# Kernel tuning notes

Hardware: AMD Instinct MI355X
Metric: run time of the kernel (lower is better)

Reference implementation:

```python
import jax, jax.numpy as jnp
import numpy as np

N_NODES = 50000
N_EDGES = 1600000
IN_DIM, HID_DIM, OUT_DIM = 512, 256, 128
N_IDX = 8192


def _graph_conv(x, src, dst, W, b, n_nodes):
    # DGL GraphConv, norm='both': D_dst^{-1/2} A D_src^{-1/2} x W + b
    ones = jnp.ones(src.shape[0], dtype=x.dtype)
    deg_out = jax.ops.segment_sum(ones, src, num_segments=n_nodes)
    deg_in = jax.ops.segment_sum(ones, dst, num_segments=n_nodes)
    ns = jax.lax.rsqrt(jnp.maximum(deg_out, 1.0))  # source norm
    nd = jax.lax.rsqrt(jnp.maximum(deg_in, 1.0))   # dest norm
    msg = (x * ns[:, None])[src]                   # gather [E, F]
    agg = jax.ops.segment_sum(msg, dst, num_segments=n_nodes)
    return (agg * nd[:, None]) @ W + b


def _gcn(x, src, dst, W1, b1, W2, b2, n_nodes):
    h = jax.nn.relu(_graph_conv(x, src, dst, W1, b1, n_nodes))
    return _graph_conv(h, src, dst, W2, b2, n_nodes)


def setup_inputs() -> dict:
    key = jax.random.key(0)
    ks = jax.random.split(key, 16)
    d = {
        'raw1': jax.random.normal(ks[0], (N_NODES, IN_DIM), jnp.float32),
        'raw2': jax.random.normal(ks[1], (N_NODES, IN_DIM), jnp.float32),
        'src1': jax.random.randint(ks[2], (N_EDGES,), 0, N_NODES),
        'dst1': jax.random.randint(ks[3], (N_EDGES,), 0, N_NODES),
        'src2': jax.random.randint(ks[4], (N_EDGES,), 0, N_NODES),
        'dst2': jax.random.randint(ks[5], (N_EDGES,), 0, N_NODES),
        'index': jax.random.randint(ks[6], (N_IDX,), 0, N_NODES),
    }
    def lin(k, fi, fo):
        s = 1.0 / np.sqrt(fi)
        return jax.random.uniform(k, (fi, fo), jnp.float32, -s, s)
    d['e1_W1'] = lin(ks[7], IN_DIM, HID_DIM); d['e1_b1'] = jnp.zeros(HID_DIM, jnp.float32)
    d['e1_W2'] = lin(ks[8], HID_DIM, OUT_DIM); d['e1_b2'] = jnp.zeros(OUT_DIM, jnp.float32)
    d['e2_W1'] = lin(ks[9], IN_DIM, HID_DIM); d['e2_b1'] = jnp.zeros(HID_DIM, jnp.float32)
    d['e2_W2'] = lin(ks[10], HID_DIM, OUT_DIM); d['e2_b2'] = jnp.zeros(OUT_DIM, jnp.float32)
    return d


def reference(raw1, raw2, src1, dst1, src2, dst2, index,
              e1_W1, e1_b1, e1_W2, e1_b2, e2_W1, e2_b1, e2_W2, e2_b2):
    n = raw1.shape[0]
    c1 = _gcn(raw1, src1, dst1, e1_W1, e1_b1, e1_W2, e1_b2, n)[index]
    c2 = _gcn(raw2, src2, dst2, e2_W1, e2_b1, e2_W2, e2_b2, n)[index]
    # F.normalize(dim=1), eps=1e-12
    c1 = c1 / jnp.maximum(jnp.linalg.norm(c1, axis=1, keepdims=True), 1e-12)
    c2 = c2 / jnp.maximum(jnp.linalg.norm(c2, axis=1, keepdims=True), 1e-12)
    z1 = c1 @ c1.T
    z2 = c2 @ c2.T
    z3 = c1 @ c2.T
    z3 = (z3 + z3.T) * 0.5
    z = (z1 + z2 + z3) * (1.0 / 3.0)
    return jnp.triu(z)
```

## Files before the change

### kernel.cpp

```cpp
#include <hip/hip_runtime.h>
#include <hip/hip_bf16.h>

using u16 = unsigned short;
using u32 = unsigned int;

typedef __attribute__((ext_vector_type(8))) short short8;
typedef __attribute__((ext_vector_type(4))) float f32x4;

__device__ __forceinline__ u16 f2bf_u16(float f) {
    __hip_bfloat16 h = __float2bfloat16(f);
    return __builtin_bit_cast(u16, h);
}
__device__ __forceinline__ float bfu(u32 u) { return __uint_as_float(u << 16); }

static constexpr int NN = 50000;
static constexpr int NE = 1600000;
static constexpr int NIDX = 8192;
static constexpr int NRANGE = 8;
static constexpr int RN = NN / NRANGE;
static constexpr int HCH = 16;
static constexpr int NK = NN * NRANGE;
static constexpr int SAB = (NK + 4095) / 4096;
static constexpr int CAPB = 262144;
static constexpr int PEB = 8192;
static constexpr int PGX = (NE + PEB - 1) / PEB;
static constexpr int PSTG = 1536;
static constexpr int ZLB = 64 * 63 / 2;
static constexpr int ZHB = ZLB / 2;
static constexpr int ZUB = 64 * 65 / 2;
static constexpr int AGB = NN / 4;


__global__ __launch_bounds__(256)
void partition_kernel(const int* __restrict__ s1, const int* __restrict__ d1,
                      const int* __restrict__ s2, const int* __restrict__ d2,
                      int* __restrict__ bcur, u32* __restrict__ ebuf_d, u16* __restrict__ ebuf_s) {
    __shared__ u32 stage_d[8][PSTG];
    __shared__ u16 stage_s[8][PSTG];
    __shared__ int cnt_d[8], cnt_s[8], base_d[8], base_s[8];
    int enc = blockIdx.y;
    const int* s = enc ? s2 : s1;
    const int* d = enc ? d2 : d1;
    if (threadIdx.x < 8) { cnt_d[threadIdx.x] = 0; cnt_s[threadIdx.x] = 0; }
    __syncthreads();
    int* bc_d = bcur + enc * 16;
    int* bc_s = bcur + enc * 16 + 8;
    u32* bd = ebuf_d + (size_t)enc * 8 * CAPB;
    u16* bs = ebuf_s + (size_t)enc * 8 * CAPB;
    int e0 = blockIdx.x * PEB;
    int e1 = min(e0 + PEB, NE);
    for (int e = e0 + threadIdx.x * 4; e < e1; e += 1024) {
        int4 sv = *(const int4*)(s + e);
        int4 dv = *(const int4*)(d + e);
        #pragma unroll
        for (int j = 0; j < 4; ++j) {
            int src = j == 0 ? sv.x : j == 1 ? sv.y : j == 2 ? sv.z : sv.w;
            int dst = j == 0 ? dv.x : j == 1 ? dv.y : j == 2 ? dv.z : dv.w;
            int rd = dst / RN;
            u32 entry = (u32)src | ((u32)(dst - rd * RN) << 16);
            int slot = atomicAdd(&cnt_d[rd], 1);
            if (slot < PSTG) stage_d[rd][slot] = entry;
            else { int gp = atomicAdd(&bc_d[rd], 1); bd[(size_t)rd * CAPB + gp] = entry; }
            int rs = src / RN;
            int slot2 = atomicAdd(&cnt_s[rs], 1);
            if (slot2 < PSTG) stage_s[rs][slot2] = (u16)(src - rs * RN);
            else { int gp = atomicAdd(&bc_s[rs], 1); bs[(size_t)rs * CAPB + gp] = (u16)(src - rs * RN); }
        }
    }
    __syncthreads();
    if (threadIdx.x < 8) {
        int b = threadIdx.x;
        base_d[b] = atomicAdd(&bc_d[b], min(cnt_d[b], PSTG));
        base_s[b] = atomicAdd(&bc_s[b], min(cnt_s[b], PSTG));
    }
    __syncthreads();
    #pragma unroll
    for (int b = 0; b < 8; ++b) {
        int nb = min(cnt_d[b], PSTG);
        for (int i = threadIdx.x; i < nb; i += 256)
            bd[(size_t)b * CAPB + base_d[b] + i] = stage_d[b][i];
        int ns = min(cnt_s[b], PSTG);
        for (int i = threadIdx.x; i < ns; i += 256)
            bs[(size_t)b * CAPB + base_s[b] + i] = stage_s[b][i];
    }
}


__global__ __launch_bounds__(256)
void bhist_kernel(const u32* __restrict__ ebuf_d, const u16* __restrict__ ebuf_s,
                  const int* __restrict__ bcur,
                  u32* __restrict__ partial2, u32* __restrict__ partial_out) {
    __shared__ u32 sh[RN * 2];
    int stripe = blockIdx.x & 7, chunk = blockIdx.x >> 3;
    int enc = blockIdx.y & 1, type = blockIdx.y >> 1;
    if (type == 0) {
        for (int i = threadIdx.x; i < RN * 2; i += 256) sh[i] = 0;
        __syncthreads();
        int size = bcur[enc * 16 + stripe];
        int cs = (size + HCH - 1) / HCH;
        int lo = chunk * cs, hi = min(lo + cs, size);
        const u32* b = ebuf_d + ((size_t)enc * 8 + stripe) * CAPB;
        for (int i = lo + threadIdx.x; i < hi; i += 256) {
            u32 e = b[i];
            u32 idx = (e >> 16) * 8 + (e & 0xffffu) / RN;
            atomicAdd(&sh[idx >> 2], 1u << ((idx & 3) * 8));
        }
        __syncthreads();
        u32* p2 = partial2 + ((size_t)enc * HCH + chunk) * (NN * 2) + stripe * (RN * 2);
        for (int i = threadIdx.x; i < RN * 2; i += 256) p2[i] = sh[i];
    } else {
        for (int i = threadIdx.x; i < RN / 2; i += 256) sh[i] = 0;
        __syncthreads();
        int size = bcur[enc * 16 + 8 + stripe];
        int cs = (size + HCH - 1) / HCH;
        int lo = chunk * cs, hi = min(lo + cs, size);
        const u16* b = ebuf_s + ((size_t)enc * 8 + stripe) * CAPB;
        for (int i = lo + threadIdx.x; i < hi; i += 256) {
            u32 sl = b[i];
            atomicAdd(&sh[sl >> 1], 1u << ((sl & 1) * 16));
        }
        __syncthreads();
        u32* po = partial_out + ((size_t)enc * HCH + chunk) * (NN / 2) + stripe * (RN / 2);
        for (int i = threadIdx.x; i < RN / 2; i += 256) po[i] = sh[i];
    }
}

__global__ void reduce_hist_kernel(const u32* __restrict__ partial2,
                                   const u32* __restrict__ partial_out,
                                   int* __restrict__ deg2, float* __restrict__ norms) {
    int i = blockIdx.x * blockDim.x + threadIdx.x;
    if (i >= 2 * NN) return;
    int enc = i / NN;
    int dst = i - enc * NN;
    int cnt[8];
    #pragma unroll
    for (int r = 0; r < 8; ++r) cnt[r] = 0;
    for (int c = 0; c < HCH; ++c) {
        const u32* p = partial2 + ((size_t)enc * HCH + c) * (NN * 2) + dst * 2;
        u32 w0 = p[0], w1 = p[1];
        cnt[0] += w0 & 0xff; cnt[1] += (w0 >> 8) & 0xff; cnt[2] += (w0 >> 16) & 0xff; cnt[3] += w0 >> 24;
        cnt[4] += w1 & 0xff; cnt[5] += (w1 >> 8) & 0xff; cnt[6] += (w1 >> 16) & 0xff; cnt[7] += w1 >> 24;
    }
    int* dp = deg2 + (size_t)enc * NK + dst * 8;
    int din = 0;
    #pragma unroll
    for (int r = 0; r < 8; ++r) { dp[r] = cnt[r]; din += cnt[r]; }
    norms[(enc * 2 + 1) * NN + dst] = rsqrtf(fmaxf((float)din, 1.f));
    int dout = 0;
    for (int c = 0; c < HCH; ++c) {
        u32 w = partial_out[((size_t)enc * HCH + c) * (NN / 2) + (dst >> 1)];
        dout += (w >> ((dst & 1) * 16)) & 0xffff;
    }
    norms[(enc * 2 + 0) * NN + dst] = rsqrtf(fmaxf((float)dout, 1.f));
}


__global__ __launch_bounds__(1024)
void scanA_kernel(const int* __restrict__ deg2, int* __restrict__ rp2_all, int* __restrict__ tot) {
    int enc = blockIdx.y;
    const int* deg = deg2 + (size_t)enc * NK;
    int* rp = rp2_all + (size_t)enc * (NK + 1);
    __shared__ int wsum[16];
    int t = threadIdx.x, lane = t & 63, wid = t >> 6;
    int i0 = blockIdx.x * 4096 + t * 4;
    int4 v = make_int4(0, 0, 0, 0);
    bool in = (i0 + 3 < NK);
    if (in) v = *(const int4*)(deg + i0);
    int s = v.x + v.y + v.z + v.w;
    int x = s;
    #pragma unroll
    for (int d = 1; d < 64; d <<= 1) {
        int y = __shfl_up(x, d, 64);
        if (lane >= d) x += y;
    }
    if (lane == 63) wsum[wid] = x;
    __syncthreads();
    if (t == 0) {
        int run = 0;
        #pragma unroll
        for (int w = 0; w < 16; ++w) { int q = wsum[w]; wsum[w] = run; run += q; }
        tot[enc * SAB + blockIdx.x] = run;
    }
    __syncthreads();
    if (in) {
        int excl = wsum[wid] + x - s;
        rp[i0] = excl;
        rp[i0 + 1] = excl + v.x;
        rp[i0 + 2] = excl + v.x + v.y;
        rp[i0 + 3] = excl + v.x + v.y + v.z;
    }
}

__global__ __launch_bounds__(256)
void scanC_kernel(int* __restrict__ rp2_all, int* __restrict__ cur2_all, const int* __restrict__ tot) {
    int enc = blockIdx.y;
    int* rp = rp2_all + (size_t)enc * (NK + 1);
    int* cur = cur2_all + (size_t)enc * NK;
    int nA = blockIdx.x >> 2;
    int part = 0;
    for (int i = threadIdx.x; i < nA; i += 256) part += tot[enc * SAB + i];
    #pragma unroll
    for (int d = 1; d < 64; d <<= 1) part += __shfl_xor(part, d, 64);
    __shared__ int red[4];
    __shared__ int soff;
    int lane = threadIdx.x & 63, wv = threadIdx.x >> 6;
    if (lane == 0) red[wv] = part;
    __syncthreads();
    if (threadIdx.x == 0) soff = red[0] + red[1] + red[2] + red[3];
    __syncthreads();
    int off = soff;
    int idx = (blockIdx.x * 256 + threadIdx.x) * 4;
    if (idx < NK) {
        int4 v = *(const int4*)(rp + idx);
        v.x += off; v.y += off; v.z += off; v.w += off;
        *(int4*)(rp + idx) = v;
        *(int4*)(cur + idx) = v;
    }
    if (blockIdx.x == 0 && threadIdx.x == 0) rp[NK] = NE;
}


__global__ __launch_bounds__(256)
void scatter_kernel(const u32* __restrict__ ebuf_d, const int* __restrict__ bcur,
                    int* __restrict__ cur2_all, u16* __restrict__ csr_all) {
    int stripe = blockIdx.x & 7, chunk = blockIdx.x >> 3;
    int enc = blockIdx.y;
    int size = bcur[enc * 16 + stripe];
    int cs = (size + 63) / 64;
    int lo = chunk * cs, hi = min(lo + cs, size);
    const u32* b = ebuf_d + ((size_t)enc * 8 + stripe) * CAPB;
    int* cursor = cur2_all + (size_t)enc * NK;
    u16* csr = csr_all + (size_t)enc * NE;
    int base = stripe * RN;
    for (int i = lo + threadIdx.x; i < hi; i += 256) {
        u32 e = b[i];
        int src = e & 0xffff;
        int dst = base + (int)(e >> 16);
        int key = dst * 8 + src / RN;
        int pos = atomicAdd(&cursor[key], 1);
        csr[pos] = (u16)src;
    }
}

__global__ void convw_kernel(const float* __restrict__ W1a, const float* __restrict__ W1b,
                             const float* __restrict__ W2a, const float* __restrict__ W2b,
                             u16* __restrict__ W1t_all, u16* __restrict__ W2t_all) {
    int mat = blockIdx.y;
    int idx = blockIdx.x * blockDim.x + threadIdx.x;
    const float* W; u16* Wt; int K, N;
    if (mat < 2) { W = mat ? W1b : W1a; Wt = W1t_all + (size_t)mat * 512 * 256; K = 512; N = 256; }
    else         { W = (mat == 3) ? W2b : W2a; Wt = W2t_all + (size_t)(mat - 2) * 256 * 128; K = 256; N = 128; }
    if (idx < K * N) {
        int k = idx / N, n = idx - k * N;
        Wt[(size_t)n * K + k] = f2bf_u16(W[idx]);
    }
}


template<bool A_F32, bool OUT_BF16, bool TRIANG, bool SCALE>
__global__ __launch_bounds__(256)
void gemm_kernel(const void* __restrict__ A0_, const void* __restrict__ A1_,
                 const u16* __restrict__ Bt0, const u16* __restrict__ Bt1,
                 void* __restrict__ C0_, void* __restrict__ C1_,
                 const float* __restrict__ rs0, const float* __restrict__ rs1,
                 int M, int N, int K) {
    int enc = blockIdx.z;
    const void* A_ = enc ? A1_ : A0_;
    const u16* Bt = enc ? Bt1 : Bt0;
    void* C_ = enc ? C1_ : C0_;
    const float* rowscale = enc ? rs1 : rs0;

    int it, jt;
    if (TRIANG) {
        int b = blockIdx.x;
        int i = (int)((129.0f - sqrtf(129.f * 129.f - 8.f * b)) * 0.5f);
        while ((i + 1) * (129 - (i + 1)) / 2 <= b) ++i;
        while (i * (129 - i) / 2 > b) --i;
        it = i;
        jt = i + (b - i * (129 - i) / 2);
    } else {
        it = blockIdx.x; jt = blockIdx.y;
    }
    int t = threadIdx.x;
    int brow = it * 128, bcol = jt * 128;
    float* Cf = (float*)C_;
    __shared__ alignas(16) u16 smem[128 * 40 * 2];
    u16* As = smem;
    u16* Bs = smem + 128 * 40;
    int lane = t & 63, wv = t >> 6;
    int wr = wv >> 1, wc = wv & 1;
    f32x4 acc[4][4];
    #pragma unroll
    for (int m = 0; m < 4; ++m)
        #pragma unroll
        for (int n = 0; n < 4; ++n) acc[m][n] = f32x4{0.f, 0.f, 0.f, 0.f};

    float4 a_f0[4], a_f1[4];
    uint4  a_h0[2], a_h1[2];
    uint4  b_h0[2], b_h1[2];

#define LOADT(S, kk) do {                                                          \
    if constexpr (A_F32) {                                                         \
        const float* A = (const float*)A_;                                         \
        _Pragma("unroll")                                                          \
        for (int p = 0; p < 4; ++p) {                                              \
            int r = p * 32 + (t >> 3), c = (t & 7) * 4;                            \
            int gr = brow + r;                                                     \
            a_f##S[p] = make_float4(0.f, 0.f, 0.f, 0.f);                           \
            if (gr < M) a_f##S[p] = *(const float4*)(A + (size_t)gr * K + (kk) + c); \
        }                                                                          \
    } else {                                                                       \
        const u16* A = (const u16*)A_;                                             \
        _Pragma("unroll")                                                          \
        for (int p = 0; p < 2; ++p) {                                              \
            int r = p * 64 + (t >> 2), c = (t & 3) * 8;                            \
            int gr = brow + r;                                                     \
            a_h##S[p] = make_uint4(0u, 0u, 0u, 0u);                                \
            if (gr < M) a_h##S[p] = *(const uint4*)(A + (size_t)gr * K + (kk) + c); \
        }                                                                          \
    }                                                                              \
    _Pragma("unroll")                                                              \
    for (int p = 0; p < 2; ++p) {                                                  \
        int r = p * 64 + (t >> 2), c = (t & 3) * 8;                                \
        int gn = bcol + r;                                                         \
        b_h##S[p] = make_uint4(0u, 0u, 0u, 0u);                                    \
        if (gn < N) b_h##S[p] = *(const uint4*)(Bt + (size_t)gn * K + (kk) + c);   \
    }                                                                              \
} while (0)

#define STORET(S) do {                                                             \
    if constexpr (A_F32) {                                                         \
        _Pragma("unroll")                                                          \
        for (int p = 0; p < 4; ++p) {                                              \
            int r = p * 32 + (t >> 3), c = (t & 7) * 4;                            \
            u32 lo = (u32)f2bf_u16(a_f##S[p].x) | ((u32)f2bf_u16(a_f##S[p].y) << 16); \
            u32 hi = (u32)f2bf_u16(a_f##S[p].z) | ((u32)f2bf_u16(a_f##S[p].w) << 16); \
            *(uint2*)&As[r * 40 + c] = make_uint2(lo, hi);                         \
        }                                                                          \
    } else {                                                                       \
        _Pragma("unroll")                                                          \
        for (int p = 0; p < 2; ++p) {                                              \
            int r = p * 64 + (t >> 2), c = (t & 3) * 8;                            \
            *(uint4*)&As[r * 40 + c] = a_h##S[p];                                  \
        }                                                                          \
    }                                                                              \
    _Pragma("unroll")                                                              \
    for (int p = 0; p < 2; ++p) {                                                  \
        int r = p * 64 + (t >> 2), c = (t & 3) * 8;                                \
        *(uint4*)&Bs[r * 40 + c] = b_h##S[p];                                      \
    }                                                                              \
} while (0)

    auto compute = [&]() {
        int kg = (lane >> 4) * 8;
        short8 av[4], bv[4];
        #pragma unroll
        for (int m = 0; m < 4; ++m)
            av[m] = *(const short8*)&As[(wr * 64 + m * 16 + (lane & 15)) * 40 + kg];
        #pragma unroll
        for (int n = 0; n < 4; ++n)
            bv[n] = *(const short8*)&Bs[(wc * 64 + n * 16 + (lane & 15)) * 40 + kg];
        #pragma unroll
        for (int m = 0; m < 4; ++m)
            #pragma unroll
            for (int n = 0; n < 4; ++n)
                acc[m][n] = __builtin_amdgcn_mfma_f32_16x16x32_bf16(av[m], bv[n], acc[m][n], 0, 0, 0);
    };

    LOADT(0, 0);
    LOADT(1, 32);
    for (int k0 = 0; k0 < K; k0 += 64) {
        STORET(0);
        __syncthreads();
        if (k0 + 64 < K) LOADT(0, k0 + 64);
        compute();
        __syncthreads();
        STORET(1);
        __syncthreads();
        if (k0 + 96 < K) LOADT(1, k0 + 96);
        compute();
        __syncthreads();
    }
#undef LOADT
#undef STORET

    const int lane15 = lane & 15, lanehi = lane >> 4;
    if (OUT_BF16) {
        u16* stg = smem + wv * 1024;
        #pragma unroll
        for (int m = 0; m < 4; ++m) {
            #pragma unroll
            for (int n = 0; n < 4; ++n)
                #pragma unroll
                for (int r = 0; r < 4; ++r) {
                    float v = acc[m][n][r];
                    if (SCALE) v *= rowscale[brow + wr * 64 + m * 16 + lanehi * 4 + r];
                    stg[(lanehi * 4 + r) * 64 + n * 16 + lane15] = f2bf_u16(v);
                }
            #pragma unroll
            for (int pass = 0; pass < 2; ++pass) {
                int lr = pass * 8 + (lane >> 3);
                int grow = brow + wr * 64 + m * 16 + lr;
                uint4 w = *(uint4*)&stg[lr * 64 + (lane & 7) * 8];
                if (grow < M)
                    *(uint4*)((u16*)C_ + (size_t)grow * N + bcol + wc * 64 + (lane & 7) * 8) = w;
            }
        }
    } else {
        float* stg = (float*)smem + wv * 1024;
        #pragma unroll
        for (int m = 0; m < 4; ++m) {
            #pragma unroll
            for (int n = 0; n < 4; ++n)
                #pragma unroll
                for (int r = 0; r < 4; ++r) {
                    int row = brow + wr * 64 + m * 16 + lanehi * 4 + r;
                    int col = bcol + wc * 64 + n * 16 + lane15;
                    float v = acc[m][n][r];
                    if (SCALE) v *= rowscale[row];
                    if (TRIANG && col < row) v = 0.f;
                    stg[(lanehi * 4 + r) * 64 + n * 16 + lane15] = v;
                }
            #pragma unroll
            for (int pass = 0; pass < 4; ++pass) {
                int lr = pass * 4 + lanehi;
                int grow = brow + wr * 64 + m * 16 + lr;
                f32x4 w = *(f32x4*)&stg[lr * 64 + lane15 * 4];
                if (grow < M) {
                    float* dp = Cf + (size_t)grow * N + bcol + wc * 64 + lane15 * 4;
                    if (TRIANG) __builtin_nontemporal_store(w, (f32x4*)dp);
                    else *(f32x4*)dp = w;
                }
            }
        }
    }
}


template<int F, bool RELU, bool OUT_BF16, bool ZFILL>
__global__ __launch_bounds__(256)
void agg_kernel(const u16* __restrict__ Yall, const int* __restrict__ rp2_all,
                const u16* __restrict__ csr_all, const float* __restrict__ norms,
                const float* __restrict__ bias0, const float* __restrict__ bias1,
                void* __restrict__ out_all, float* __restrict__ zout) {
    constexpr int VPL = F / 64;
    int enc = blockIdx.y;
    int bid = blockIdx.x;
    if (ZFILL) {
        if (bid < ZHB) {
            int b = enc * ZHB + bid;
            float fit = (sqrtf(8.f * b + 1.f) + 1.f) * 0.5f;
            int it = (int)fit;
            if (it * (it - 1) / 2 > b) --it;
            else if ((it + 1) * it / 2 <= b) ++it;
            int jt = b - it * (it - 1) / 2;
            int brow = it * 128, bcol = jt * 128;
            f32x4 z = {0.f, 0.f, 0.f, 0.f};
            #pragma unroll
            for (int pq = 0; pq < 16; ++pq) {
                int idx = pq * 256 + threadIdx.x;
                int r = idx >> 5, c4 = idx & 31;
                __builtin_nontemporal_store(z, (f32x4*)(zout + (size_t)(brow + r) * NIDX + bcol + c4 * 4));
            }
            return;
        }
        bid -= ZHB;
    }
    const u16* Y = Yall + (size_t)enc * NN * F;
    const int* rp2 = rp2_all + (size_t)enc * (NK + 1);
    const u16* csr = csr_all + (size_t)enc * NE;
    const float* nd = norms + (size_t)(2 * enc + 1) * NN;
    const float* bias = enc ? bias1 : bias0;
    int lane = threadIdx.x & 63;
    int node = bid * 4 + (threadIdx.x >> 6);
    int e0 = rp2[node * 8], e1 = rp2[node * 8 + 8];
    float acc[VPL];
    #pragma unroll
    for (int j = 0; j < VPL; ++j) acc[j] = 0.f;
    const int off = lane * VPL;

    int e = e0;
    for (; e < e1 && (e & 7) != 0; ++e) {
        int s = csr[e];
        if (VPL == 4) {
            uint2 d = *(const uint2*)(Y + (size_t)s * F + off);
            acc[0] += bfu(d.x & 0xffffu); acc[1] += bfu(d.x >> 16);
            acc[2] += bfu(d.y & 0xffffu); acc[3] += bfu(d.y >> 16);
        } else {
            u32 d = *(const u32*)(Y + (size_t)s * F + off);
            acc[0] += bfu(d & 0xffffu); acc[1] += bfu(d >> 16);
        }
    }
    if (VPL == 4) {
        for (; e + 16 <= e1; e += 16) {
            uint4 ia = *(const uint4*)(csr + e);
            uint4 ib = *(const uint4*)(csr + e + 8);
            int s0 = ia.x & 0xffff, s1 = ia.x >> 16, s2 = ia.y & 0xffff, s3 = ia.y >> 16;
            int s4 = ia.z & 0xffff, s5 = ia.z >> 16, s6 = ia.w & 0xffff, s7 = ia.w >> 16;
            int s8 = ib.x & 0xffff, s9 = ib.x >> 16, sa = ib.y & 0xffff, sb = ib.y >> 16;
            int sc = ib.z & 0xffff, sd = ib.z >> 16, se = ib.w & 0xffff, sf = ib.w >> 16;
            uint2 d0 = *(const uint2*)(Y + (size_t)s0 * F + off);
            uint2 d1 = *(const uint2*)(Y + (size_t)s1 * F + off);
            uint2 d2 = *(const uint2*)(Y + (size_t)s2 * F + off);
            uint2 d3 = *(const uint2*)(Y + (size_t)s3 * F + off);
            uint2 d4 = *(const uint2*)(Y + (size_t)s4 * F + off);
            uint2 d5 = *(const uint2*)(Y + (size_t)s5 * F + off);
            uint2 d6 = *(const uint2*)(Y + (size_t)s6 * F + off);
            uint2 d7 = *(const uint2*)(Y + (size_t)s7 * F + off);
            uint2 d8 = *(const uint2*)(Y + (size_t)s8 * F + off);
            uint2 d9 = *(const uint2*)(Y + (size_t)s9 * F + off);
            uint2 da = *(const uint2*)(Y + (size_t)sa * F + off);
            uint2 db = *(const uint2*)(Y + (size_t)sb * F + off);
            uint2 dc = *(const uint2*)(Y + (size_t)sc * F + off);
            uint2 dd = *(const uint2*)(Y + (size_t)sd * F + off);
            uint2 de = *(const uint2*)(Y + (size_t)se * F + off);
            uint2 df = *(const uint2*)(Y + (size_t)sf * F + off);
            acc[0] += bfu(d0.x & 0xffffu); acc[1] += bfu(d0.x >> 16); acc[2] += bfu(d0.y & 0xffffu); acc[3] += bfu(d0.y >> 16);
            acc[0] += bfu(d1.x & 0xffffu); acc[1] += bfu(d1.x >> 16); acc[2] += bfu(d1.y & 0xffffu); acc[3] += bfu(d1.y >> 16);
            acc[0] += bfu(d2.x & 0xffffu); acc[1] += bfu(d2.x >> 16); acc[2] += bfu(d2.y & 0xffffu); acc[3] += bfu(d2.y >> 16);
            acc[0] += bfu(d3.x & 0xffffu); acc[1] += bfu(d3.x >> 16); acc[2] += bfu(d3.y & 0xffffu); acc[3] += bfu(d3.y >> 16);
            acc[0] += bfu(d4.x & 0xffffu); acc[1] += bfu(d4.x >> 16); acc[2] += bfu(d4.y & 0xffffu); acc[3] += bfu(d4.y >> 16);
            acc[0] += bfu(d5.x & 0xffffu); acc[1] += bfu(d5.x >> 16); acc[2] += bfu(d5.y & 0xffffu); acc[3] += bfu(d5.y >> 16);
            acc[0] += bfu(d6.x & 0xffffu); acc[1] += bfu(d6.x >> 16); acc[2] += bfu(d6.y & 0xffffu); acc[3] += bfu(d6.y >> 16);
            acc[0] += bfu(d7.x & 0xffffu); acc[1] += bfu(d7.x >> 16); acc[2] += bfu(d7.y & 0xffffu); acc[3] += bfu(d7.y >> 16);
            acc[0] += bfu(d8.x & 0xffffu); acc[1] += bfu(d8.x >> 16); acc[2] += bfu(d8.y & 0xffffu); acc[3] += bfu(d8.y >> 16);
            acc[0] += bfu(d9.x & 0xffffu); acc[1] += bfu(d9.x >> 16); acc[2] += bfu(d9.y & 0xffffu); acc[3] += bfu(d9.y >> 16);
            acc[0] += bfu(da.x & 0xffffu); acc[1] += bfu(da.x >> 16); acc[2] += bfu(da.y & 0xffffu); acc[3] += bfu(da.y >> 16);
            acc[0] += bfu(db.x & 0xffffu); acc[1] += bfu(db.x >> 16); acc[2] += bfu(db.y & 0xffffu); acc[3] += bfu(db.y >> 16);
            acc[0] += bfu(dc.x & 0xffffu); acc[1] += bfu(dc.x >> 16); acc[2] += bfu(dc.y & 0xffffu); acc[3] += bfu(dc.y >> 16);
            acc[0] += bfu(dd.x & 0xffffu); acc[1] += bfu(dd.x >> 16); acc[2] += bfu(dd.y & 0xffffu); acc[3] += bfu(dd.y >> 16);
            acc[0] += bfu(de.x & 0xffffu); acc[1] += bfu(de.x >> 16); acc[2] += bfu(de.y & 0xffffu); acc[3] += bfu(de.y >> 16);
            acc[0] += bfu(df.x & 0xffffu); acc[1] += bfu(df.x >> 16); acc[2] += bfu(df.y & 0xffffu); acc[3] += bfu(df.y >> 16);
        }
    }
    for (; e + 8 <= e1; e += 8) {
        uint4 iv = *(const uint4*)(csr + e);
        int s0 = iv.x & 0xffff, s1 = iv.x >> 16;
        int s2 = iv.y & 0xffff, s3 = iv.y >> 16;
        int s4 = iv.z & 0xffff, s5 = iv.z >> 16;
        int s6 = iv.w & 0xffff, s7 = iv.w >> 16;
        if (VPL == 4) {
            uint2 d0 = *(const uint2*)(Y + (size_t)s0 * F + off);
            uint2 d1 = *(const uint2*)(Y + (size_t)s1 * F + off);
            uint2 d2 = *(const uint2*)(Y + (size_t)s2 * F + off);
            uint2 d3 = *(const uint2*)(Y + (size_t)s3 * F + off);
            uint2 d4 = *(const uint2*)(Y + (size_t)s4 * F + off);
            uint2 d5 = *(const uint2*)(Y + (size_t)s5 * F + off);
            uint2 d6 = *(const uint2*)(Y + (size_t)s6 * F + off);
            uint2 d7 = *(const uint2*)(Y + (size_t)s7 * F + off);
            acc[0] += bfu(d0.x & 0xffffu); acc[1] += bfu(d0.x >> 16); acc[2] += bfu(d0.y & 0xffffu); acc[3] += bfu(d0.y >> 16);
            acc[0] += bfu(d1.x & 0xffffu); acc[1] += bfu(d1.x >> 16); acc[2] += bfu(d1.y & 0xffffu); acc[3] += bfu(d1.y >> 16);
            acc[0] += bfu(d2.x & 0xffffu); acc[1] += bfu(d2.x >> 16); acc[2] += bfu(d2.y & 0xffffu); acc[3] += bfu(d2.y >> 16);
            acc[0] += bfu(d3.x & 0xffffu); acc[1] += bfu(d3.x >> 16); acc[2] += bfu(d3.y & 0xffffu); acc[3] += bfu(d3.y >> 16);
            acc[0] += bfu(d4.x & 0xffffu); acc[1] += bfu(d4.x >> 16); acc[2] += bfu(d4.y & 0xffffu); acc[3] += bfu(d4.y >> 16);
            acc[0] += bfu(d5.x & 0xffffu); acc[1] += bfu(d5.x >> 16); acc[2] += bfu(d5.y & 0xffffu); acc[3] += bfu(d5.y >> 16);
            acc[0] += bfu(d6.x & 0xffffu); acc[1] += bfu(d6.x >> 16); acc[2] += bfu(d6.y & 0xffffu); acc[3] += bfu(d6.y >> 16);
            acc[0] += bfu(d7.x & 0xffffu); acc[1] += bfu(d7.x >> 16); acc[2] += bfu(d7.y & 0xffffu); acc[3] += bfu(d7.y >> 16);
        } else {
            u32 d0 = *(const u32*)(Y + (size_t)s0 * F + off);
            u32 d1 = *(const u32*)(Y + (size_t)s1 * F + off);
            u32 d2 = *(const u32*)(Y + (size_t)s2 * F + off);
            u32 d3 = *(const u32*)(Y + (size_t)s3 * F + off);
            u32 d4 = *(const u32*)(Y + (size_t)s4 * F + off);
            u32 d5 = *(const u32*)(Y + (size_t)s5 * F + off);
            u32 d6 = *(const u32*)(Y + (size_t)s6 * F + off);
            u32 d7 = *(const u32*)(Y + (size_t)s7 * F + off);
            acc[0] += bfu(d0 & 0xffffu); acc[1] += bfu(d0 >> 16);
            acc[0] += bfu(d1 & 0xffffu); acc[1] += bfu(d1 >> 16);
            acc[0] += bfu(d2 & 0xffffu); acc[1] += bfu(d2 >> 16);
            acc[0] += bfu(d3 & 0xffffu); acc[1] += bfu(d3 >> 16);
            acc[0] += bfu(d4 & 0xffffu); acc[1] += bfu(d4 >> 16);
            acc[0] += bfu(d5 & 0xffffu); acc[1] += bfu(d5 >> 16);
            acc[0] += bfu(d6 & 0xffffu); acc[1] += bfu(d6 >> 16);
            acc[0] += bfu(d7 & 0xffffu); acc[1] += bfu(d7 >> 16);
        }
    }
    for (; e < e1; ++e) {
        int s = csr[e];
        if (VPL == 4) {
            uint2 d = *(const uint2*)(Y + (size_t)s * F + off);
            acc[0] += bfu(d.x & 0xffffu); acc[1] += bfu(d.x >> 16);
            acc[2] += bfu(d.y & 0xffffu); acc[3] += bfu(d.y >> 16);
        } else {
            u32 d = *(const u32*)(Y + (size_t)s * F + off);
            acc[0] += bfu(d & 0xffffu); acc[1] += bfu(d >> 16);
        }
    }

    float ndv = nd[node];
    #pragma unroll
    for (int j = 0; j < VPL; ++j) {
        float o = acc[j] * ndv + bias[off + j];
        if (RELU) o = fmaxf(o, 0.f);
        if (OUT_BF16) ((u16*)out_all)[(size_t)enc * NN * F + (size_t)node * F + off + j] = f2bf_u16(o);
        else ((float*)out_all)[(size_t)enc * NN * F + (size_t)node * F + off + j] = o;
    }
}


__global__ __launch_bounds__(256)
void build_r_kernel(const float* __restrict__ H2a, const float* __restrict__ H2b,
                    const int* __restrict__ index, u16* __restrict__ R) {
    int lane = threadIdx.x & 63;
    int row = blockIdx.x * 4 + (threadIdx.x >> 6);
    int g = index[row];
    float2 a = *(const float2*)(H2a + (size_t)g * 128 + lane * 2);
    float2 b = *(const float2*)(H2b + (size_t)g * 128 + lane * 2);
    float sa = a.x * a.x + a.y * a.y;
    float sb = b.x * b.x + b.y * b.y;
    #pragma unroll
    for (int d = 1; d < 64; d <<= 1) {
        sa += __shfl_xor(sa, d, 64);
        sb += __shfl_xor(sb, d, 64);
    }
    float inva = 1.f / fmaxf(sqrtf(sa), 1e-12f);
    float invb = 1.f / fmaxf(sqrtf(sb), 1e-12f);
    float ax = a.x * inva, ay = a.y * inva;
    float bx = b.x * invb, by = b.y * invb;
    const float c2 = 0.5f, c3 = 0.28867513459481287f;
    u16* Rp = R + (size_t)row * 256;
    Rp[lane * 2]           = f2bf_u16((ax + bx) * c2);
    Rp[lane * 2 + 1]       = f2bf_u16((ay + by) * c2);
    Rp[128 + lane * 2]     = f2bf_u16((ax - bx) * c3);
    Rp[128 + lane * 2 + 1] = f2bf_u16((ay - by) * c3);
}


extern "C" void kernel_launch(void* const* d_in, const int* in_sizes, int n_in,
                              void* d_out, int out_size, void* d_ws, size_t ws_size,
                              hipStream_t stream) {
    (void)in_sizes; (void)n_in; (void)out_size; (void)ws_size;
    const float* raw0 = (const float*)d_in[0];
    const float* raw1 = (const float*)d_in[1];
    const int* src1 = (const int*)d_in[2], *dst1 = (const int*)d_in[3];
    const int* src2 = (const int*)d_in[4], *dst2 = (const int*)d_in[5];
    const int* index = (const int*)d_in[6];
    const float* W1a = (const float*)d_in[7];  const float* b1a = (const float*)d_in[8];
    const float* W2a = (const float*)d_in[9];  const float* b2a = (const float*)d_in[10];
    const float* W1b = (const float*)d_in[11]; const float* b1b = (const float*)d_in[12];
    const float* W2b = (const float*)d_in[13]; const float* b2b = (const float*)d_in[14];

    char* wp = (char*)d_ws;
    auto alloc = [&](size_t bytes) -> char* {
        char* r = wp;
        wp += (bytes + 255) & ~(size_t)255;
        return r;
    };
    float* norms   = (float*)alloc((size_t)4 * NN * 4);
    int*   deg2    = (int*)alloc((size_t)2 * NK * 4);
    int*   rp2     = (int*)alloc((size_t)2 * (NK + 1) * 4);
    int*   cur2    = (int*)alloc((size_t)2 * NK * 4);
    int*   tot     = (int*)alloc((size_t)2 * SAB * 4);
    int*   bcur    = (int*)alloc(32 * 4);
    u16*   csr_all = (u16*)alloc((size_t)2 * NE * 2);
    u16*   W1t     = (u16*)alloc((size_t)2 * 512 * 256 * 2);
    u16*   W2t     = (u16*)alloc((size_t)2 * 256 * 128 * 2);
    u16*   Y1      = (u16*)alloc((size_t)2 * NN * 256 * 2);
    u16*   H1      = (u16*)alloc((size_t)2 * NN * 256 * 2);
    u16*   Y2      = (u16*)alloc((size_t)2 * NN * 128 * 2);
    float* H2      = (float*)alloc((size_t)2 * NN * 128 * 4);
    u16*   R       = (u16*)alloc((size_t)NIDX * 256 * 2);
    u32* partial2    = (u32*)Y1;
    u32* partial_out = (u32*)H1;
    u32* ebuf_d      = (u32*)Y2;
    u16* ebuf_s      = (u16*)H2;

    const int MT = (NN + 127) / 128;

    hipMemsetAsync(bcur, 0, 32 * 4, stream);
    convw_kernel<<<dim3((512 * 256 + 255) / 256, 4), 256, 0, stream>>>(W1a, W1b, W2a, W2b, W1t, W2t);
    partition_kernel<<<dim3(PGX, 2), 256, 0, stream>>>(src1, dst1, src2, dst2, bcur, ebuf_d, ebuf_s);
    bhist_kernel<<<dim3(8 * HCH, 4), 256, 0, stream>>>(ebuf_d, ebuf_s, bcur, partial2, partial_out);
    reduce_hist_kernel<<<(2 * NN + 255) / 256, 256, 0, stream>>>(partial2, partial_out, deg2, norms);
    scanA_kernel<<<dim3(SAB, 2), 1024, 0, stream>>>(deg2, rp2, tot);
    scanC_kernel<<<dim3((NK / 4 + 255) / 256, 2), 256, 0, stream>>>(rp2, cur2, tot);
    scatter_kernel<<<dim3(8 * 64, 2), 256, 0, stream>>>(ebuf_d, bcur, cur2, csr_all);

    gemm_kernel<true, true, false, true><<<dim3(MT, 2, 2), 256, 0, stream>>>(
        raw0, raw1, W1t, W1t + (size_t)512 * 256, Y1, Y1 + (size_t)NN * 256,
        norms, norms + (size_t)2 * NN, NN, 256, 512);
    agg_kernel<256, true, true, true><<<dim3(ZHB + AGB, 2), 256, 0, stream>>>(
        Y1, rp2, csr_all, norms, b1a, b1b, H1, (float*)d_out);
    gemm_kernel<false, true, false, true><<<dim3(MT, 1, 2), 256, 0, stream>>>(
        H1, H1 + (size_t)NN * 256, W2t, W2t + (size_t)256 * 128, Y2, Y2 + (size_t)NN * 128,
        norms, norms + (size_t)2 * NN, NN, 128, 256);
    agg_kernel<128, false, false, false><<<dim3(AGB, 2), 256, 0, stream>>>(
        Y2, rp2, csr_all, norms, b2a, b2b, H2, nullptr);

    build_r_kernel<<<NIDX / 4, 256, 0, stream>>>(H2, H2 + (size_t)NN * 128, index, R);
    gemm_kernel<false, false, true, false><<<dim3(ZUB, 1, 1), 256, 0, stream>>>(
        R, R, R, R, (float*)d_out, (float*)d_out, nullptr, nullptr, NIDX, NIDX, 256);
}
```

Baseline: 658.9 us.

## Fold weight conversion into partition and overlap CSR scatter with first GEMM

Weight transposition/bf16 conversion now runs on extra blocks of the partition kernel, which removes one launch. The CSR scatter runs as extra blocks appended to the first-layer GEMM grid, so it overlaps with that GEMM. Those blocks claim work through an atomic ticket counter, and the memset now also zeroes the ticket counters. The scatter's atomics and writes now compete with the GEMM for bandwidth, and the GEMM is refactored into a device function used by three kernels.

```diff
diff --git a/kernel.cpp b/kernel.cpp
--- a/kernel.cpp
+++ b/kernel.cpp
@@ -24,17 +24,44 @@
 static constexpr int CAPB = 262144;
 static constexpr int PEB = 8192;
 static constexpr int PGX = (NE + PEB - 1) / PEB;
+static constexpr int CVB = 640;
 static constexpr int PSTG = 1536;
 static constexpr int ZLB = 64 * 63 / 2;
 static constexpr int ZHB = ZLB / 2;
 static constexpr int ZUB = 64 * 65 / 2;
 static constexpr int AGB = NN / 4;
+static constexpr int MT = (NN + 127) / 128;
+static constexpr int SCX = 256;
 
 
 __global__ __launch_bounds__(256)
 void partition_kernel(const int* __restrict__ s1, const int* __restrict__ d1,
                       const int* __restrict__ s2, const int* __restrict__ d2,
-                      int* __restrict__ bcur, u32* __restrict__ ebuf_d, u16* __restrict__ ebuf_s) {
+                      int* __restrict__ bcur, u32* __restrict__ ebuf_d, u16* __restrict__ ebuf_s,
+                      const float* __restrict__ W1a, const float* __restrict__ W1b,
+                      const float* __restrict__ W2a, const float* __restrict__ W2b,
+                      u16* __restrict__ W1t, u16* __restrict__ W2t) {
+    if (blockIdx.x >= PGX) {
+        int o = (blockIdx.x - PGX) + CVB * blockIdx.y;
+        int idx = o * 256 + threadIdx.x;
+        if (idx < 131072) {
+            int k = idx >> 8, n = idx & 255;
+            W1t[(size_t)n * 512 + k] = f2bf_u16(W1a[idx]);
+        } else if (idx < 262144) {
+            int j = idx - 131072;
+            int k = j >> 8, n = j & 255;
+            W1t[(size_t)131072 + (size_t)n * 512 + k] = f2bf_u16(W1b[j]);
+        } else if (idx < 294912) {
+            int j = idx - 262144;
+            int k = j >> 7, n = j & 127;
+            W2t[(size_t)n * 256 + k] = f2bf_u16(W2a[j]);
+        } else if (idx < 327680) {
+            int j = idx - 294912;
+            int k = j >> 7, n = j & 127;
+            W2t[(size_t)32768 + (size_t)n * 256 + k] = f2bf_u16(W2b[j]);
+        }
+        return;
+    }
     __shared__ u32 stage_d[8][PSTG];
     __shared__ u16 stage_s[8][PSTG];
     __shared__ int cnt_d[8], cnt_s[8], base_d[8], base_s[8];
@@ -220,11 +247,10 @@
 }
 
 
-__global__ __launch_bounds__(256)
-void scatter_kernel(const u32* __restrict__ ebuf_d, const int* __restrict__ bcur,
-                    int* __restrict__ cur2_all, u16* __restrict__ csr_all) {
-    int stripe = blockIdx.x & 7, chunk = blockIdx.x >> 3;
-    int enc = blockIdx.y;
+__device__ __forceinline__ void scatter_body(const u32* __restrict__ ebuf_d,
+                                             const int* __restrict__ bcur,
+                                             int* __restrict__ cur2_all, u16* __restrict__ csr_all,
+                                             int stripe, int chunk, int enc) {
     int size = bcur[enc * 16 + stripe];
     int cs = (size + 63) / 64;
     int lo = chunk * cs, hi = min(lo + cs, size);
@@ -242,49 +268,14 @@
     }
 }
 
-__global__ void convw_kernel(const float* __restrict__ W1a, const float* __restrict__ W1b,
-                             const float* __restrict__ W2a, const float* __restrict__ W2b,
-                             u16* __restrict__ W1t_all, u16* __restrict__ W2t_all) {
-    int mat = blockIdx.y;
-    int idx = blockIdx.x * blockDim.x + threadIdx.x;
-    const float* W; u16* Wt; int K, N;
-    if (mat < 2) { W = mat ? W1b : W1a; Wt = W1t_all + (size_t)mat * 512 * 256; K = 512; N = 256; }
-    else         { W = (mat == 3) ? W2b : W2a; Wt = W2t_all + (size_t)(mat - 2) * 256 * 128; K = 256; N = 128; }
-    if (idx < K * N) {
-        int k = idx / N, n = idx - k * N;
-        Wt[(size_t)n * K + k] = f2bf_u16(W[idx]);
-    }
-}
-
 
 template<bool A_F32, bool OUT_BF16, bool TRIANG, bool SCALE>
-__global__ __launch_bounds__(256)
-void gemm_kernel(const void* __restrict__ A0_, const void* __restrict__ A1_,
-                 const u16* __restrict__ Bt0, const u16* __restrict__ Bt1,
-                 void* __restrict__ C0_, void* __restrict__ C1_,
-                 const float* __restrict__ rs0, const float* __restrict__ rs1,
-                 int M, int N, int K) {
-    int enc = blockIdx.z;
-    const void* A_ = enc ? A1_ : A0_;
-    const u16* Bt = enc ? Bt1 : Bt0;
-    void* C_ = enc ? C1_ : C0_;
-    const float* rowscale = enc ? rs1 : rs0;
-
-    int it, jt;
-    if (TRIANG) {
-        int b = blockIdx.x;
-        int i = (int)((129.0f - sqrtf(129.f * 129.f - 8.f * b)) * 0.5f);
-        while ((i + 1) * (129 - (i + 1)) / 2 <= b) ++i;
-        while (i * (129 - i) / 2 > b) --i;
-        it = i;
-        jt = i + (b - i * (129 - i) / 2);
-    } else {
-        it = blockIdx.x; jt = blockIdx.y;
-    }
+__device__ __forceinline__ void gemm_device(const void* __restrict__ A_, const u16* __restrict__ Bt,
+                                            void* __restrict__ C_, const float* __restrict__ rowscale,
+                                            int M, int N, int K, int it, int jt, u16* smem) {
     int t = threadIdx.x;
     int brow = it * 128, bcol = jt * 128;
     float* Cf = (float*)C_;
-    __shared__ alignas(16) u16 smem[128 * 40 * 2];
     u16* As = smem;
     u16* Bs = smem + 128 * 40;
     int lane = t & 63, wv = t >> 6;
@@ -434,6 +425,53 @@
             }
         }
     }
+}
+
+__global__ __launch_bounds__(256)
+void gemm1scat_kernel(const float* __restrict__ raw0, const float* __restrict__ raw1,
+                      const u16* __restrict__ W1t, u16* __restrict__ Y1,
+                      const float* __restrict__ norms,
+                      const u32* __restrict__ ebuf_d, const int* __restrict__ bcur,
+                      int* __restrict__ tick, int* __restrict__ cur2, u16* __restrict__ csr_all) {
+    if (blockIdx.x >= MT) {
+        u32 lin = blockIdx.x + gridDim.x * (blockIdx.y + gridDim.y * blockIdx.z);
+        int stripe = lin & 7;
+        __shared__ int tsh;
+        if (threadIdx.x == 0) tsh = atomicAdd(&tick[stripe], 1);
+        __syncthreads();
+        int tkt = tsh;
+        scatter_body(ebuf_d, bcur, cur2, csr_all, stripe, tkt & 63, tkt >> 6);
+        return;
+    }
+    __shared__ alignas(16) u16 smem[128 * 40 * 2];
+    int enc = blockIdx.z;
+    gemm_device<true, true, false, true>(
+        enc ? raw1 : raw0, W1t + (size_t)enc * 512 * 256,
+        Y1 + (size_t)enc * NN * 256, norms + (size_t)2 * enc * NN,
+        NN, 256, 512, blockIdx.x, blockIdx.y, smem);
+}
+
+__global__ __launch_bounds__(256)
+void gemm2_kernel(const u16* __restrict__ H1, const u16* __restrict__ W2t,
+                  u16* __restrict__ Y2, const float* __restrict__ norms) {
+    __shared__ alignas(16) u16 smem[128 * 40 * 2];
+    int enc = blockIdx.z;
+    gemm_device<false, true, false, true>(
+        H1 + (size_t)enc * NN * 256, W2t + (size_t)enc * 256 * 128,
+        Y2 + (size_t)enc * NN * 128, norms + (size_t)2 * enc * NN,
+        NN, 128, 256, blockIdx.x, 0, smem);
+}
+
+__global__ __launch_bounds__(256)
+void zgemm_kernel(const u16* __restrict__ R, float* __restrict__ out) {
+    int b = blockIdx.x;
+    int i = (int)((129.0f - sqrtf(129.f * 129.f - 8.f * b)) * 0.5f);
+    while ((i + 1) * (129 - (i + 1)) / 2 <= b) ++i;
+    while (i * (129 - i) / 2 > b) --i;
+    int it = i;
+    int jt = i + (b - i * (129 - i) / 2);
+    __shared__ alignas(16) u16 smem[128 * 40 * 2];
+    gemm_device<false, false, true, false>(R, R, out, nullptr, NIDX, NIDX, 256, it, jt, smem);
 }
 
 
@@ -651,7 +689,7 @@
     int*   rp2     = (int*)alloc((size_t)2 * (NK + 1) * 4);
     int*   cur2    = (int*)alloc((size_t)2 * NK * 4);
     int*   tot     = (int*)alloc((size_t)2 * SAB * 4);
-    int*   bcur    = (int*)alloc(32 * 4);
+    int*   bcur    = (int*)alloc(48 * 4);
     u16*   csr_all = (u16*)alloc((size_t)2 * NE * 2);
     u16*   W1t     = (u16*)alloc((size_t)2 * 512 * 256 * 2);
     u16*   W2t     = (u16*)alloc((size_t)2 * 256 * 128 * 2);
@@ -660,34 +698,28 @@
     u16*   Y2      = (u16*)alloc((size_t)2 * NN * 128 * 2);
     float* H2      = (float*)alloc((size_t)2 * NN * 128 * 4);
     u16*   R       = (u16*)alloc((size_t)NIDX * 256 * 2);
+    int*   tick    = bcur + 32;
     u32* partial2    = (u32*)Y1;
     u32* partial_out = (u32*)H1;
     u32* ebuf_d      = (u32*)Y2;
     u16* ebuf_s      = (u16*)H2;
 
-    const int MT = (NN + 127) / 128;
-
-    hipMemsetAsync(bcur, 0, 32 * 4, stream);
-    convw_kernel<<<dim3((512 * 256 + 255) / 256, 4), 256, 0, stream>>>(W1a, W1b, W2a, W2b, W1t, W2t);
-    partition_kernel<<<dim3(PGX, 2), 256, 0, stream>>>(src1, dst1, src2, dst2, bcur, ebuf_d, ebuf_s);
+    hipMemsetAsync(bcur, 0, 48 * 4, stream);
+    partition_kernel<<<dim3(PGX + CVB, 2), 256, 0, stream>>>(
+        src1, dst1, src2, dst2, bcur, ebuf_d, ebuf_s, W1a, W1b, W2a, W2b, W1t, W2t);
     bhist_kernel<<<dim3(8 * HCH, 4), 256, 0, stream>>>(ebuf_d, ebuf_s, bcur, partial2, partial_out);
     reduce_hist_kernel<<<(2 * NN + 255) / 256, 256, 0, stream>>>(partial2, partial_out, deg2, norms);
     scanA_kernel<<<dim3(SAB, 2), 1024, 0, stream>>>(deg2, rp2, tot);
     scanC_kernel<<<dim3((NK / 4 + 255) / 256, 2), 256, 0, stream>>>(rp2, cur2, tot);
-    scatter_kernel<<<dim3(8 * 64, 2), 256, 0, stream>>>(ebuf_d, bcur, cur2, csr_all);
-
-    gemm_kernel<true, true, false, true><<<dim3(MT, 2, 2), 256, 0, stream>>>(
-        raw0, raw1, W1t, W1t + (size_t)512 * 256, Y1, Y1 + (size_t)NN * 256,
-        norms, norms + (size_t)2 * NN, NN, 256, 512);
+
+    gemm1scat_kernel<<<dim3(MT + SCX, 2, 2), 256, 0, stream>>>(
+        raw0, raw1, W1t, Y1, norms, ebuf_d, bcur, tick, cur2, csr_all);
     agg_kernel<256, true, true, true><<<dim3(ZHB + AGB, 2), 256, 0, stream>>>(
         Y1, rp2, csr_all, norms, b1a, b1b, H1, (float*)d_out);
-    gemm_kernel<false, true, false, true><<<dim3(MT, 1, 2), 256, 0, stream>>>(
-        H1, H1 + (size_t)NN * 256, W2t, W2t + (size_t)256 * 128, Y2, Y2 + (size_t)NN * 128,
-        norms, norms + (size_t)2 * NN, NN, 128, 256);
+    gemm2_kernel<<<dim3(MT, 1, 2), 256, 0, stream>>>(H1, W2t, Y2, norms);
     agg_kernel<128, false, false, false><<<dim3(AGB, 2), 256, 0, stream>>>(
         Y2, rp2, csr_all, norms, b2a, b2b, H2, nullptr);
 
     build_r_kernel<<<NIDX / 4, 256, 0, stream>>>(H2, H2 + (size_t)NN * 128, index, R);
-    gemm_kernel<false, false, true, false><<<dim3(ZUB, 1, 1), 256, 0, stream>>>(
-        R, R, R, R, (float*)d_out, (float*)d_out, nullptr, nullptr, NIDX, NIDX, 256);
-}
+    zgemm_kernel<<<dim3(ZUB, 1, 1), 256, 0, stream>>>(R, (float*)d_out);
+}
```

New measurement: 624.0 us. -5.3%, faster.
